# Kernel tuning notes

Measured on AMD Instinct MI355X. Metric: run time of the kernel, lower is better.

The kernel has to match this reference:

```python
import jax, jax.numpy as jnp
import numpy as np

N = 50000      # nodes
E = 800000     # edges (avg degree 16)
NF, EF, H, OUT, K = 16, 8, 64, 8, 3
N_MID = 2      # n_gnn_layers=4 -> first + 2 mid + last


def setup_inputs() -> dict:
    key = jax.random.key(0)
    ks = jax.random.split(key, 16)
    s = 0.05
    return {
        "x": jax.random.normal(ks[0], (N, NF), dtype=jnp.float32),
        "edge_index": jax.random.randint(ks[1], (2, E), 0, N, dtype=jnp.int64),
        "edge_attr": jax.random.normal(ks[2], (E, EF), dtype=jnp.float32),
        # edge_aggr MLP: Linear(EF,H) -> ReLU -> Linear(H,1)
        "mlp_W1": jax.random.normal(ks[3], (EF, H), dtype=jnp.float32) * s,
        "mlp_b1": jnp.zeros((H,), dtype=jnp.float32),
        "mlp_W2": jax.random.normal(ks[4], (H, 1), dtype=jnp.float32) * s,
        "mlp_b2": jnp.zeros((1,), dtype=jnp.float32),
        # TAGConv-style layers: K+1 linear maps each
        "W_first": jax.random.normal(ks[5], (K + 1, NF, H), dtype=jnp.float32) * s,
        "b_first": jnp.zeros((H,), dtype=jnp.float32),
        "W_mid": jax.random.normal(ks[6], (N_MID, K + 1, H, H), dtype=jnp.float32) * s,
        "b_mid": jnp.zeros((N_MID, H), dtype=jnp.float32),
        "W_last": jax.random.normal(ks[7], (K + 1, H, OUT), dtype=jnp.float32) * s,
        "b_last": jnp.zeros((OUT,), dtype=jnp.float32),
    }


def _gcn_norm(edge_weight, src, dst, n_nodes):
    # deg computed at target (col), D^{-1/2} A D^{-1/2}, no self loops
    deg = jax.ops.segment_sum(edge_weight, dst, num_segments=n_nodes)
    dinv = jnp.where(deg > 0, jax.lax.rsqrt(jnp.where(deg > 0, deg, 1.0)), 0.0)
    return dinv[src] * edge_weight * dinv[dst]  # [E]


def _tag_conv(x, Ws, b, src, dst, norm, n_nodes):
    # out = sum_k (A_norm^k x) W_k + b
    out = x @ Ws[0]
    h = x
    for k in range(1, Ws.shape[0]):
        h = jax.ops.segment_sum(h[src] * norm[:, None], dst, num_segments=n_nodes)
        out = out + h @ Ws[k]
    return out + b


def reference(x, edge_index, edge_attr, mlp_W1, mlp_b1, mlp_W2, mlp_b2,
              W_first, b_first, W_mid, b_mid, W_last, b_last):
    src, dst = edge_index[0], edge_index[1]
    n_nodes = x.shape[0]
    # edge MLP -> scalar edge weight per edge
    ew = (jax.nn.relu(edge_attr @ mlp_W1 + mlp_b1) @ mlp_W2 + mlp_b2)[:, 0]  # [E]
    norm = _gcn_norm(ew, src, dst, n_nodes)
    h = jax.nn.relu(_tag_conv(x, W_first, b_first, src, dst, norm, n_nodes))
    for i in range(W_mid.shape[0]):
        h = jax.nn.relu(_tag_conv(h, W_mid[i], b_mid[i], src, dst, norm, n_nodes))
    return _tag_conv(h, W_last, b_last, src, dst, norm, n_nodes)
```

## Files before the change

kernel.cpp:

```cpp
#include <hip/hip_runtime.h>
#include <stdint.h>

#define N_NODES 50000
#define N_EDGES 800000
#define NFEAT   16
#define EFEAT   8
#define HID     64
#define OUTF    8
#define NMID    2
#define NX      (N_NODES * NFEAT)
#define NPW     16
#define CAP     64
#define PGB     ((N_NODES + 4 * NPW - 1) / (4 * NPW))
#define PPB     ((N_NODES + 15) / 16)
#define NWB     ((N_NODES + 3) / 4)

typedef unsigned short ushort_t;
typedef unsigned int   uint_t;
typedef unsigned long long ull_t;
typedef __bf16 bf16x8 __attribute__((ext_vector_type(8)));
typedef float  f32x4  __attribute__((ext_vector_type(4)));

__device__ __forceinline__ float b2f(ushort_t u) {
    return __uint_as_float(((uint_t)u) << 16);
}
__device__ __forceinline__ ushort_t f2b(float f) {
    uint_t u = __float_as_uint(f);
    return (ushort_t)((u + 0x7fffu + ((u >> 16) & 1u)) >> 16);
}

__global__ __launch_bounds__(256) void edge_mlp_kernel(
    const float* __restrict__ ea, const float* __restrict__ x,
    const int* __restrict__ ei,
    const float* __restrict__ W1, const float* __restrict__ b1,
    const float* __restrict__ W2, const float* __restrict__ b2,
    ushort_t* __restrict__ xb, int* __restrict__ cnts, ull_t* __restrict__ bucket)
{
    __shared__ float W1s[EFEAT * HID];
    __shared__ float b1s[HID];
    __shared__ float W2s[HID];
    __shared__ float b2s;
    int tid = threadIdx.x;
    for (int i = tid; i < EFEAT * HID; i += 256) W1s[i] = W1[i];
    if (tid < HID) { b1s[tid] = b1[tid]; W2s[tid] = W2[tid]; }
    if (tid == 0) b2s = b2[0];
    __syncthreads();

    int base = (blockIdx.x * 256 + tid) * 4;
    if (base >= N_EDGES) return;

    float4 xv = ((const float4*)x)[base >> 2];
    xb[base + 0] = f2b(xv.x); xb[base + 1] = f2b(xv.y);
    xb[base + 2] = f2b(xv.z); xb[base + 3] = f2b(xv.w);

    float a[4][8];
    #pragma unroll
    for (int k = 0; k < 4; ++k) {
        float4 v0 = ((const float4*)ea)[2 * (base + k)];
        float4 v1 = ((const float4*)ea)[2 * (base + k) + 1];
        a[k][0]=v0.x; a[k][1]=v0.y; a[k][2]=v0.z; a[k][3]=v0.w;
        a[k][4]=v1.x; a[k][5]=v1.y; a[k][6]=v1.z; a[k][7]=v1.w;
    }

    float acc0 = b2s, acc1 = b2s, acc2 = b2s, acc3 = b2s;
    #pragma unroll 4
    for (int j = 0; j < HID; ++j) {
        float h0 = b1s[j], h1 = b1s[j], h2 = b1s[j], h3 = b1s[j];
        #pragma unroll
        for (int i = 0; i < EFEAT; ++i) {
            float w = W1s[i * HID + j];
            h0 = fmaf(a[0][i], w, h0);
            h1 = fmaf(a[1][i], w, h1);
            h2 = fmaf(a[2][i], w, h2);
            h3 = fmaf(a[3][i], w, h3);
        }
        float w2 = W2s[j];
        acc0 = fmaf(fmaxf(h0, 0.f), w2, acc0);
        acc1 = fmaf(fmaxf(h1, 0.f), w2, acc1);
        acc2 = fmaf(fmaxf(h2, 0.f), w2, acc2);
        acc3 = fmaf(fmaxf(h3, 0.f), w2, acc3);
    }
    float accs[4] = {acc0, acc1, acc2, acc3};

    int4 sv = ((const int4*)ei)[base >> 2];
    int4 dv = ((const int4*)(ei + N_EDGES))[base >> 2];
    int ss[4] = {sv.x, sv.y, sv.z, sv.w};
    int dd[4] = {dv.x, dv.y, dv.z, dv.w};
    #pragma unroll
    for (int k = 0; k < 4; ++k) {
        int pos = atomicAdd(&cnts[dd[k]], 1);
        if (pos < CAP)
            bucket[(size_t)dd[k] * CAP + pos] =
                (((ull_t)__float_as_uint(accs[k])) << 32) | (uint_t)ss[k];
    }
}

__global__ __launch_bounds__(256) void degdinv_kernel(
    int* __restrict__ cnts, const ull_t* __restrict__ bucket,
    float* __restrict__ dinv)
{
    int tid = threadIdx.x;
    int n = blockIdx.x * 4 + (tid >> 6);
    int lane = tid & 63;
    if (n >= N_NODES) return;
    int c = cnts[n]; if (c > CAP) c = CAP;
    float w = 0.f;
    if (lane < c)
        w = __uint_as_float((uint_t)(bucket[(size_t)n * CAP + lane] >> 32));
    #pragma unroll
    for (int o = 32; o; o >>= 1) w += __shfl_down(w, o, 64);
    if (lane == 0) {
        cnts[n] = c;
        dinv[n] = (w > 0.f) ? (1.f / sqrtf(w)) : 0.f;
    }
}

__global__ __launch_bounds__(256) void rescale_kernel(
    const int* __restrict__ cnts, const float* __restrict__ dinv,
    ull_t* __restrict__ bucket)
{
    int tid = threadIdx.x;
    int n = blockIdx.x * 4 + (tid >> 6);
    int lane = tid & 63;
    if (n >= N_NODES) return;
    int c = cnts[n];
    float dn = dinv[n];
    if (lane < c) {
        ull_t p = bucket[(size_t)n * CAP + lane];
        uint_t src = (uint_t)p;
        float w = __uint_as_float((uint_t)(p >> 32));
        float nv = dinv[src] * w * dn;
        bucket[(size_t)n * CAP + lane] = (((ull_t)__float_as_uint(nv)) << 32) | src;
    }
}

template<int W>
__global__ __launch_bounds__(256, 6) void prop_kernel(
    const ushort_t* __restrict__ gsrc, ushort_t* __restrict__ gout,
    const int* __restrict__ cnts, const ull_t* __restrict__ bucket)
{
    int tid = threadIdx.x;
    int wv = tid >> 6, lane = tid & 63;
    int nb = (blockIdx.x * 4 + wv) * 4;
    if (nb >= N_NODES) return;

    int cv = (lane < 4) ? cnts[nb + lane] : 0;
    int c0 = __builtin_amdgcn_readlane(cv, 0);
    int c1 = __builtin_amdgcn_readlane(cv, 1);
    int c2 = __builtin_amdgcn_readlane(cv, 2);
    int c3 = __builtin_amdgcn_readlane(cv, 3);

    ull_t b0 = 0, b1 = 0, b2 = 0, b3 = 0;
    if (lane < c0) b0 = bucket[(size_t)(nb + 0) * CAP + lane];
    if (lane < c1) b1 = bucket[(size_t)(nb + 1) * CAP + lane];
    if (lane < c2) b2 = bucket[(size_t)(nb + 2) * CAP + lane];
    if (lane < c3) b3 = bucket[(size_t)(nb + 3) * CAP + lane];
    uint_t ms0 = (uint_t)b0, mn0 = (uint_t)(b0 >> 32);
    uint_t ms1 = (uint_t)b1, mn1 = (uint_t)(b1 >> 32);
    uint_t ms2 = (uint_t)b2, mn2 = (uint_t)(b2 >> 32);
    uint_t ms3 = (uint_t)b3, mn3 = (uint_t)(b3 >> 32);

    if (W == 64) {
        float s[4][4];
        #pragma unroll
        for (int n = 0; n < 4; ++n)
            #pragma unroll
            for (int k = 0; k < 4; ++k) s[n][k] = 0.f;

        int cq0 = c0 & ~3, cq1 = c1 & ~3, cq2 = c2 & ~3, cq3 = c3 & ~3;
        int cqm = max(max(cq0, cq1), max(cq2, cq3));

        for (int j = 0; j < cqm; j += 4) {
            #define GATHER4(msN, mnN, cqN, n)                                        \
                if (j < cqN) {                                                       \
                    _Pragma("unroll")                                                \
                    for (int k = 0; k < 4; ++k) {                                    \
                        int   si = __builtin_amdgcn_readlane((int)msN, j + k);       \
                        float nv = __uint_as_float(                                  \
                            (uint_t)__builtin_amdgcn_readlane((int)mnN, j + k));     \
                        float h = b2f(gsrc[(size_t)si * 64 + lane]);                 \
                        s[n][k] = fmaf(h, nv, s[n][k]);                              \
                    }                                                                \
                }
            GATHER4(ms0, mn0, cq0, 0)
            GATHER4(ms1, mn1, cq1, 1)
            GATHER4(ms2, mn2, cq2, 2)
            GATHER4(ms3, mn3, cq3, 3)
            #undef GATHER4
        }
        #define TAIL(msN, mnN, cqN, cN, n)                                           \
            for (int j = cqN; j < cN; ++j) {                                         \
                int   si = __builtin_amdgcn_readlane((int)msN, j);                   \
                float nv = __uint_as_float(                                          \
                    (uint_t)__builtin_amdgcn_readlane((int)mnN, j));                 \
                float h = b2f(gsrc[(size_t)si * 64 + lane]);                         \
                s[n][0] = fmaf(h, nv, s[n][0]);                                      \
            }
        TAIL(ms0, mn0, cq0, c0, 0)
        TAIL(ms1, mn1, cq1, c1, 1)
        TAIL(ms2, mn2, cq2, c2, 2)
        TAIL(ms3, mn3, cq3, c3, 3)
        #undef TAIL

        #pragma unroll
        for (int n = 0; n < 4; ++n) {
            float v = (s[n][0] + s[n][1]) + (s[n][2] + s[n][3]);
            gout[(size_t)(nb + n) * 64 + lane] = f2b(v);
        }
    } else {
        const int il = lane & 15;
        const int quad = lane >> 4;
        #define PROC16(msN, mnN, cN, n)                                              \
            {                                                                        \
                float s = 0.f;                                                       \
                for (int j = 0; j < cN; j += 4) {                                    \
                    int j4 = j + quad;                                               \
                    int sw = __shfl((int)msN, j4 & 63, 64);                          \
                    int nw = __shfl((int)mnN, j4 & 63, 64);                          \
                    bool valid = j4 < cN;                                            \
                    int src = valid ? sw : 0;                                        \
                    float nv = valid ? __uint_as_float((uint_t)nw) : 0.f;            \
                    float h = b2f(gsrc[(size_t)src * 16 + il]);                      \
                    s = fmaf(h, nv, s);                                              \
                }                                                                    \
                s += __shfl_xor(s, 16, 64);                                          \
                s += __shfl_xor(s, 32, 64);                                          \
                if (lane < 16) gout[(size_t)(nb + n) * 16 + lane] = f2b(s);          \
            }
        PROC16(ms0, mn0, c0, 0)
        PROC16(ms1, mn1, c1, 1)
        PROC16(ms2, mn2, c2, 2)
        PROC16(ms3, mn3, c3, 3)
        #undef PROC16
    }
}

template<int SRCW, int COUT, int ACT, int F32OUT>
__global__ __launch_bounds__(256, 4) void gemm4_kernel(
    const ushort_t* __restrict__ s0, const ushort_t* __restrict__ s1,
    const ushort_t* __restrict__ s2, const ushort_t* __restrict__ s3,
    const float* __restrict__ Wg,
    const float* __restrict__ bias,
    ushort_t* __restrict__ outb, float* __restrict__ outf)
{
    constexpr int NCH = (SRCW == 16) ? 2 : 8;
    constexpr int NT  = (COUT + 15) / 16;
    __shared__ __align__(16) ushort_t Bp[NCH * NT * 512];

    int tid = threadIdx.x;
    for (int idx = tid; idx < NCH * NT * 512; idx += 256) {
        int f = idx >> 9;
        int l = (idx >> 3) & 63, j = idx & 7;
        int ch = f / NT, nt = f - ch * NT;
        int kk = ((l >> 4) << 3) + j;
        int n = nt * 16 + (l & 15);
        int widx, krow;
        if (SRCW == 16) { widx = 2 * ch + (kk >> 4); krow = kk & 15; }
        else            { widx = ch >> 1;            krow = ((ch & 1) << 5) + kk; }
        float v = (n < COUT) ? Wg[((size_t)widx * SRCW + krow) * COUT + n] : 0.f;
        Bp[idx] = f2b(v);
    }
    __syncthreads();

    int wv = tid >> 6, lane = tid & 63;
    int node_base = (blockIdx.x * 4 + wv) * NPW;
    if (node_base >= N_NODES) return;
    int m = lane & 15, quad = lane >> 4;

    const ushort_t* srcs[4] = {s0, s1, s2, s3};
    bf16x8 a[NCH];
    #pragma unroll
    for (int ch = 0; ch < NCH; ++ch) {
        const ushort_t* sp;
        size_t off;
        if (SRCW == 16) {
            sp = (quad < 2) ? srcs[2 * ch] : srcs[2 * ch + 1];
            off = (size_t)(node_base + m) * 16 + (quad & 1) * 8;
        } else {
            sp = srcs[ch >> 1];
            off = (size_t)(node_base + m) * 64 + ((ch & 1) << 5) + quad * 8;
        }
        a[ch] = *(const bf16x8*)(sp + off);
    }

    #pragma unroll
    for (int nt = 0; nt < NT; ++nt) {
        float bv = bias[(nt * 16 + m) & (COUT - 1)];
        f32x4 c = {bv, bv, bv, bv};
        #pragma unroll
        for (int ch = 0; ch < NCH; ++ch) {
            bf16x8 b = *(const bf16x8*)&Bp[((ch * NT + nt) * 64 + lane) * 8];
            c = __builtin_amdgcn_mfma_f32_16x16x32_bf16(a[ch], b, c, 0, 0, 0);
        }
        #pragma unroll
        for (int r = 0; r < 4; ++r) {
            int row = node_base + quad * 4 + r;
            if (F32OUT) {
                if (m < COUT) outf[(size_t)row * COUT + m] = c[r];
            } else {
                float v = ACT ? fmaxf(c[r], 0.f) : c[r];
                outb[(size_t)row * COUT + nt * 16 + m] = f2b(v);
            }
        }
    }
}

extern "C" void kernel_launch(void* const* d_in, const int* in_sizes, int n_in,
                              void* d_out, int out_size, void* d_ws, size_t ws_size,
                              hipStream_t stream)
{
    const float* x  = (const float*)d_in[0];
    const int*   ei = (const int*)d_in[1];
    const float* ea = (const float*)d_in[2];
    const float* W1 = (const float*)d_in[3];
    const float* b1 = (const float*)d_in[4];
    const float* W2 = (const float*)d_in[5];
    const float* b2 = (const float*)d_in[6];
    const float* Wf = (const float*)d_in[7];
    const float* bf = (const float*)d_in[8];
    const float* Wm = (const float*)d_in[9];
    const float* bm = (const float*)d_in[10];
    const float* Wl = (const float*)d_in[11];
    const float* bl = (const float*)d_in[12];

    char* ws = (char*)d_ws;
    size_t off = 0;
    auto take = [&](size_t bytes) -> char* {
        char* p = ws + off;
        off = (off + bytes + 255) & ~(size_t)255;
        return p;
    };
    int*      cnts   = (int*)take((size_t)N_NODES * 4);
    float*    dinv   = (float*)take((size_t)N_NODES * 4);
    ull_t*    bucket = (ull_t*)take((size_t)N_NODES * CAP * 8);
    ushort_t* xb     = (ushort_t*)take((size_t)NX * 2 + 256);
    ushort_t* g1     = (ushort_t*)take((size_t)N_NODES * HID * 2 + 256);
    ushort_t* g2     = (ushort_t*)take((size_t)N_NODES * HID * 2 + 256);
    ushort_t* g3     = (ushort_t*)take((size_t)N_NODES * HID * 2 + 256);
    ushort_t* curA   = (ushort_t*)take((size_t)N_NODES * HID * 2 + 256);
    ushort_t* curB   = (ushort_t*)take((size_t)N_NODES * HID * 2 + 256);

    hipMemsetAsync(cnts, 0, (size_t)N_NODES * 4, stream);

    const int EB4 = (N_EDGES + 1023) / 1024;

    edge_mlp_kernel<<<EB4, 256, 0, stream>>>(ea, x, ei, W1, b1, W2, b2, xb, cnts, bucket);
    degdinv_kernel<<<NWB, 256, 0, stream>>>(cnts, bucket, dinv);
    rescale_kernel<<<NWB, 256, 0, stream>>>(cnts, dinv, bucket);

    prop_kernel<NFEAT><<<PPB, 256, 0, stream>>>(xb, g1, cnts, bucket);
    prop_kernel<NFEAT><<<PPB, 256, 0, stream>>>(g1, g2, cnts, bucket);
    prop_kernel<NFEAT><<<PPB, 256, 0, stream>>>(g2, g3, cnts, bucket);
    gemm4_kernel<NFEAT, HID, 1, 0><<<PGB, 256, 0, stream>>>(
        xb, g1, g2, g3, Wf, bf, curA, nullptr);

    ushort_t* cin = curA;
    ushort_t* cot = curB;
    for (int L = 0; L < NMID; ++L) {
        prop_kernel<HID><<<PPB, 256, 0, stream>>>(cin, g1, cnts, bucket);
        prop_kernel<HID><<<PPB, 256, 0, stream>>>(g1, g2, cnts, bucket);
        prop_kernel<HID><<<PPB, 256, 0, stream>>>(g2, g3, cnts, bucket);
        gemm4_kernel<HID, HID, 1, 0><<<PGB, 256, 0, stream>>>(
            cin, g1, g2, g3, Wm + (size_t)L * 4 * HID * HID, bm + L * HID, cot, nullptr);
        ushort_t* t = cin; cin = cot; cot = t;
    }

    prop_kernel<HID><<<PPB, 256, 0, stream>>>(cin, g1, cnts, bucket);
    prop_kernel<HID><<<PPB, 256, 0, stream>>>(g1, g2, cnts, bucket);
    prop_kernel<HID><<<PPB, 256, 0, stream>>>(g2, g3, cnts, bucket);
    gemm4_kernel<HID, OUTF, 0, 1><<<PGB, 256, 0, stream>>>(
        cin, g1, g2, g3, Wl, bl, nullptr, (float*)d_out);
}
```

Before: 498.1 us.

## Reassociate last TAGConv layer via Horner scheme to propagate 8-wide features

The last layer now first projects the 64-wide hidden state through all four weight matrices into a 32-wide buffer, then evaluates the sum as A(A(A z3 + z2) + z1) + z0 with three 8-wide propagations instead of three 64-wide ones. This sharply cuts gather bandwidth in the final layer, at the cost of extra bf16 rounding on intermediate sums. The edge MLP kernel is also changed from four edges per thread to one edge per thread, launching four times as many threads.

```diff
diff --git a/kernel.cpp b/kernel.cpp
--- a/kernel.cpp
+++ b/kernel.cpp
@@ -46,53 +46,29 @@
     if (tid == 0) b2s = b2[0];
     __syncthreads();
 
-    int base = (blockIdx.x * 256 + tid) * 4;
-    if (base >= N_EDGES) return;
-
-    float4 xv = ((const float4*)x)[base >> 2];
-    xb[base + 0] = f2b(xv.x); xb[base + 1] = f2b(xv.y);
-    xb[base + 2] = f2b(xv.z); xb[base + 3] = f2b(xv.w);
-
-    float a[4][8];
-    #pragma unroll
-    for (int k = 0; k < 4; ++k) {
-        float4 v0 = ((const float4*)ea)[2 * (base + k)];
-        float4 v1 = ((const float4*)ea)[2 * (base + k) + 1];
-        a[k][0]=v0.x; a[k][1]=v0.y; a[k][2]=v0.z; a[k][3]=v0.w;
-        a[k][4]=v1.x; a[k][5]=v1.y; a[k][6]=v1.z; a[k][7]=v1.w;
-    }
-
-    float acc0 = b2s, acc1 = b2s, acc2 = b2s, acc3 = b2s;
+    int e = blockIdx.x * 256 + tid;
+    if (e >= N_EDGES) return;
+
+    xb[e] = f2b(x[e]);
+
+    float4 v0 = ((const float4*)ea)[2 * e];
+    float4 v1 = ((const float4*)ea)[2 * e + 1];
+    float a[8] = {v0.x, v0.y, v0.z, v0.w, v1.x, v1.y, v1.z, v1.w};
+
+    float acc = b2s;
     #pragma unroll 4
     for (int j = 0; j < HID; ++j) {
-        float h0 = b1s[j], h1 = b1s[j], h2 = b1s[j], h3 = b1s[j];
-        #pragma unroll
-        for (int i = 0; i < EFEAT; ++i) {
-            float w = W1s[i * HID + j];
-            h0 = fmaf(a[0][i], w, h0);
-            h1 = fmaf(a[1][i], w, h1);
-            h2 = fmaf(a[2][i], w, h2);
-            h3 = fmaf(a[3][i], w, h3);
-        }
-        float w2 = W2s[j];
-        acc0 = fmaf(fmaxf(h0, 0.f), w2, acc0);
-        acc1 = fmaf(fmaxf(h1, 0.f), w2, acc1);
-        acc2 = fmaf(fmaxf(h2, 0.f), w2, acc2);
-        acc3 = fmaf(fmaxf(h3, 0.f), w2, acc3);
-    }
-    float accs[4] = {acc0, acc1, acc2, acc3};
-
-    int4 sv = ((const int4*)ei)[base >> 2];
-    int4 dv = ((const int4*)(ei + N_EDGES))[base >> 2];
-    int ss[4] = {sv.x, sv.y, sv.z, sv.w};
-    int dd[4] = {dv.x, dv.y, dv.z, dv.w};
-    #pragma unroll
-    for (int k = 0; k < 4; ++k) {
-        int pos = atomicAdd(&cnts[dd[k]], 1);
-        if (pos < CAP)
-            bucket[(size_t)dd[k] * CAP + pos] =
-                (((ull_t)__float_as_uint(accs[k])) << 32) | (uint_t)ss[k];
-    }
+        float h = b1s[j];
+        #pragma unroll
+        for (int i = 0; i < EFEAT; ++i) h = fmaf(a[i], W1s[i * HID + j], h);
+        acc = fmaf(fmaxf(h, 0.f), W2s[j], acc);
+    }
+
+    int s = ei[e], d = ei[N_EDGES + e];
+    int pos = atomicAdd(&cnts[d], 1);
+    if (pos < CAP)
+        bucket[(size_t)d * CAP + pos] =
+            (((ull_t)__float_as_uint(acc)) << 32) | (uint_t)s;
 }
 
 __global__ __launch_bounds__(256) void degdinv_kernel(
@@ -235,13 +211,71 @@
     }
 }
 
-template<int SRCW, int COUT, int ACT, int F32OUT>
+template<int F32OUT>
+__global__ __launch_bounds__(256, 8) void prop8_kernel(
+    const ushort_t* __restrict__ gsrc, int GS, int GO,
+    const ushort_t* __restrict__ add, int AS, int AO,
+    ushort_t* __restrict__ outb, float* __restrict__ outf,
+    const int* __restrict__ cnts, const ull_t* __restrict__ bucket)
+{
+    int tid = threadIdx.x;
+    int wv = tid >> 6, lane = tid & 63;
+    int nb = (blockIdx.x * 4 + wv) * 4;
+    if (nb >= N_NODES) return;
+    const int oct = lane >> 3, il = lane & 7;
+
+    int cv = (lane < 4) ? cnts[nb + lane] : 0;
+    int c0 = __builtin_amdgcn_readlane(cv, 0);
+    int c1 = __builtin_amdgcn_readlane(cv, 1);
+    int c2 = __builtin_amdgcn_readlane(cv, 2);
+    int c3 = __builtin_amdgcn_readlane(cv, 3);
+
+    ull_t b0 = 0, b1 = 0, b2 = 0, b3 = 0;
+    if (lane < c0) b0 = bucket[(size_t)(nb + 0) * CAP + lane];
+    if (lane < c1) b1 = bucket[(size_t)(nb + 1) * CAP + lane];
+    if (lane < c2) b2 = bucket[(size_t)(nb + 2) * CAP + lane];
+    if (lane < c3) b3 = bucket[(size_t)(nb + 3) * CAP + lane];
+    uint_t ms0 = (uint_t)b0, mn0 = (uint_t)(b0 >> 32);
+    uint_t ms1 = (uint_t)b1, mn1 = (uint_t)(b1 >> 32);
+    uint_t ms2 = (uint_t)b2, mn2 = (uint_t)(b2 >> 32);
+    uint_t ms3 = (uint_t)b3, mn3 = (uint_t)(b3 >> 32);
+
+    #define PROC8(msN, mnN, cN, n)                                                   \
+        {                                                                            \
+            float s = 0.f;                                                           \
+            for (int j = 0; j < cN; j += 8) {                                        \
+                int jo = j + oct;                                                    \
+                int sw = __shfl((int)msN, jo & 63, 64);                              \
+                int nw = __shfl((int)mnN, jo & 63, 64);                              \
+                bool valid = jo < cN;                                                \
+                int src = valid ? sw : 0;                                            \
+                float nv = valid ? __uint_as_float((uint_t)nw) : 0.f;                \
+                float h = b2f(gsrc[(size_t)src * GS + GO + il]);                     \
+                s = fmaf(h, nv, s);                                                  \
+            }                                                                        \
+            s += __shfl_xor(s, 8, 64);                                               \
+            s += __shfl_xor(s, 16, 64);                                              \
+            s += __shfl_xor(s, 32, 64);                                              \
+            if (lane < 8) {                                                          \
+                float v = s + b2f(add[(size_t)(nb + n) * AS + AO + lane]);           \
+                if (F32OUT) outf[(size_t)(nb + n) * 8 + lane] = v;                   \
+                else        outb[(size_t)(nb + n) * 8 + lane] = f2b(v);              \
+            }                                                                        \
+        }
+    PROC8(ms0, mn0, c0, 0)
+    PROC8(ms1, mn1, c1, 1)
+    PROC8(ms2, mn2, c2, 2)
+    PROC8(ms3, mn3, c3, 3)
+    #undef PROC8
+}
+
+template<int SRCW, int COUT, int ACT>
 __global__ __launch_bounds__(256, 4) void gemm4_kernel(
     const ushort_t* __restrict__ s0, const ushort_t* __restrict__ s1,
     const ushort_t* __restrict__ s2, const ushort_t* __restrict__ s3,
     const float* __restrict__ Wg,
     const float* __restrict__ bias,
-    ushort_t* __restrict__ outb, float* __restrict__ outf)
+    ushort_t* __restrict__ outb)
 {
     constexpr int NCH = (SRCW == 16) ? 2 : 8;
     constexpr int NT  = (COUT + 15) / 16;
@@ -295,12 +329,56 @@
         #pragma unroll
         for (int r = 0; r < 4; ++r) {
             int row = node_base + quad * 4 + r;
-            if (F32OUT) {
-                if (m < COUT) outf[(size_t)row * COUT + m] = c[r];
-            } else {
-                float v = ACT ? fmaxf(c[r], 0.f) : c[r];
-                outb[(size_t)row * COUT + nt * 16 + m] = f2b(v);
-            }
+            float v = ACT ? fmaxf(c[r], 0.f) : c[r];
+            outb[(size_t)row * COUT + nt * 16 + m] = f2b(v);
+        }
+    }
+}
+
+__global__ __launch_bounds__(256, 4) void gemmL_kernel(
+    const ushort_t* __restrict__ src,
+    const float* __restrict__ Wl,
+    const float* __restrict__ bl,
+    ushort_t* __restrict__ Z)
+{
+    __shared__ __align__(16) ushort_t Bp[2 * 2 * 512];
+
+    int tid = threadIdx.x;
+    for (int idx = tid; idx < 2048; idx += 256) {
+        int f = idx >> 9;
+        int ch = f >> 1, nt = f & 1;
+        int l = (idx >> 3) & 63, j = idx & 7;
+        int kg = ch * 32 + ((l >> 4) << 3) + j;
+        int n = nt * 16 + (l & 15);
+        int widx = n >> 3, col = n & 7;
+        Bp[idx] = f2b(Wl[((size_t)widx * 64 + kg) * 8 + col]);
+    }
+    __syncthreads();
+
+    int wv = tid >> 6, lane = tid & 63;
+    int node_base = (blockIdx.x * 4 + wv) * NPW;
+    if (node_base >= N_NODES) return;
+    int m = lane & 15, quad = lane >> 4;
+
+    bf16x8 a[2];
+    #pragma unroll
+    for (int ch = 0; ch < 2; ++ch)
+        a[ch] = *(const bf16x8*)(src + (size_t)(node_base + m) * 64 + ch * 32 + quad * 8);
+
+    #pragma unroll
+    for (int nt = 0; nt < 2; ++nt) {
+        int n = nt * 16 + m;
+        float bv = (n < 8) ? bl[n] : 0.f;
+        f32x4 c = {bv, bv, bv, bv};
+        #pragma unroll
+        for (int ch = 0; ch < 2; ++ch) {
+            bf16x8 b = *(const bf16x8*)&Bp[((ch * 2 + nt) * 64 + lane) * 8];
+            c = __builtin_amdgcn_mfma_f32_16x16x32_bf16(a[ch], b, c, 0, 0, 0);
+        }
+        #pragma unroll
+        for (int r = 0; r < 4; ++r) {
+            int row = node_base + quad * 4 + r;
+            Z[(size_t)row * 32 + n] = f2b(c[r]);
         }
     }
 }
@@ -339,20 +417,23 @@
     ushort_t* g3     = (ushort_t*)take((size_t)N_NODES * HID * 2 + 256);
     ushort_t* curA   = (ushort_t*)take((size_t)N_NODES * HID * 2 + 256);
     ushort_t* curB   = (ushort_t*)take((size_t)N_NODES * HID * 2 + 256);
+    ushort_t* Z      = (ushort_t*)take((size_t)N_NODES * 32 * 2 + 256);
+    ushort_t* t8a    = (ushort_t*)take((size_t)N_NODES * 8 * 2 + 256);
+    ushort_t* t8b    = (ushort_t*)take((size_t)N_NODES * 8 * 2 + 256);
 
     hipMemsetAsync(cnts, 0, (size_t)N_NODES * 4, stream);
 
-    const int EB4 = (N_EDGES + 1023) / 1024;
-
-    edge_mlp_kernel<<<EB4, 256, 0, stream>>>(ea, x, ei, W1, b1, W2, b2, xb, cnts, bucket);
+    const int EB = (N_EDGES + 255) / 256;
+
+    edge_mlp_kernel<<<EB, 256, 0, stream>>>(ea, x, ei, W1, b1, W2, b2, xb, cnts, bucket);
     degdinv_kernel<<<NWB, 256, 0, stream>>>(cnts, bucket, dinv);
     rescale_kernel<<<NWB, 256, 0, stream>>>(cnts, dinv, bucket);
 
     prop_kernel<NFEAT><<<PPB, 256, 0, stream>>>(xb, g1, cnts, bucket);
     prop_kernel<NFEAT><<<PPB, 256, 0, stream>>>(g1, g2, cnts, bucket);
     prop_kernel<NFEAT><<<PPB, 256, 0, stream>>>(g2, g3, cnts, bucket);
-    gemm4_kernel<NFEAT, HID, 1, 0><<<PGB, 256, 0, stream>>>(
-        xb, g1, g2, g3, Wf, bf, curA, nullptr);
+    gemm4_kernel<NFEAT, HID, 1><<<PGB, 256, 0, stream>>>(
+        xb, g1, g2, g3, Wf, bf, curA);
 
     ushort_t* cin = curA;
     ushort_t* cot = curB;
@@ -360,14 +441,13 @@
         prop_kernel<HID><<<PPB, 256, 0, stream>>>(cin, g1, cnts, bucket);
         prop_kernel<HID><<<PPB, 256, 0, stream>>>(g1, g2, cnts, bucket);
         prop_kernel<HID><<<PPB, 256, 0, stream>>>(g2, g3, cnts, bucket);
-        gemm4_kernel<HID, HID, 1, 0><<<PGB, 256, 0, stream>>>(
-            cin, g1, g2, g3, Wm + (size_t)L * 4 * HID * HID, bm + L * HID, cot, nullptr);
+        gemm4_kernel<HID, HID, 1><<<PGB, 256, 0, stream>>>(
+            cin, g1, g2, g3, Wm + (size_t)L * 4 * HID * HID, bm + L * HID, cot);
         ushort_t* t = cin; cin = cot; cot = t;
     }
 
-    prop_kernel<HID><<<PPB, 256, 0, stream>>>(cin, g1, cnts, bucket);
-    prop_kernel<HID><<<PPB, 256, 0, stream>>>(g1, g2, cnts, bucket);
-    prop_kernel<HID><<<PPB, 256, 0, stream>>>(g2, g3, cnts, bucket);
-    gemm4_kernel<HID, OUTF, 0, 1><<<PGB, 256, 0, stream>>>(
-        cin, g1, g2, g3, Wl, bl, nullptr, (float*)d_out);
-}
+    gemmL_kernel<<<PGB, 256, 0, stream>>>(cin, Wl, bl, Z);
+    prop8_kernel<0><<<PPB, 256, 0, stream>>>(Z, 32, 24, Z, 32, 16, t8a, nullptr, cnts, bucket);
+    prop8_kernel<0><<<PPB, 256, 0, stream>>>(t8a, 8, 0, Z, 32, 8, t8b, nullptr, cnts, bucket);
+    prop8_kernel<1><<<PPB, 256, 0, stream>>>(t8b, 8, 0, Z, 32, 0, nullptr, (float*)d_out, cnts, bucket);
+}
```

Result: faster. 467.2 us (-6.2%).
